# Kernel tuning notes

Measured on AMD Instinct MI355X. Metric: run time of the kernel, lower is better.

Reference implementation:

```python
import jax, jax.numpy as jnp
import numpy as np

B, L, K, H = 256, 256, 128, 256


def setup_inputs() -> dict:
    key = jax.random.key(0)
    ks = jax.random.split(key, 24)

    def u(k, shape, fan):
        s = 1.0 / np.sqrt(fan)
        return jax.random.uniform(k, shape, minval=-s, maxval=s, dtype=jnp.float32)

    x = jax.random.normal(ks[0], (B, L, K), jnp.float32)
    mask = (jax.random.uniform(ks[1], (B, L, K)) < 0.7).astype(jnp.float32)
    record_num = jax.random.randint(ks[2], (B,), L // 2, L + 1)
    ts = jnp.cumsum(jax.random.uniform(ks[3], (B, L), minval=0.1, maxval=1.0, dtype=jnp.float32), axis=1)
    time_stamp = ts * (jnp.arange(L)[None, :] < record_num[:, None]).astype(jnp.float32)

    return {
        "x": x,
        "mask": mask,
        "time_stamp": time_stamp,
        # TemporalDecay h: W [H,K], stdv = 1/sqrt(out)=1/sqrt(H)
        "W_gh": u(ks[4], (H, K), H), "b_gh": u(ks[5], (H,), H),
        # TemporalDecay x (diag): W [K,K], stdv = 1/sqrt(K)
        "W_gx": u(ks[6], (K, K), K), "b_gx": u(ks[7], (K,), K),
        # hist_reg: Linear(H -> K), stdv = 1/sqrt(H)
        "W_hist": u(ks[8], (K, H), H), "b_hist": u(ks[9], (K,), H),
        "W_feat": u(ks[10], (K, K), K), "b_feat": u(ks[11], (K,), K),
        # weight_combine: Linear(2K -> K), stdv = 1/sqrt(2K)
        "W_comb": u(ks[12], (K, 2 * K), 2 * K), "b_comb": u(ks[13], (K,), 2 * K),
        # GRUCell(2K -> H): uniform 1/sqrt(H)
        "W_ih": u(ks[14], (3 * H, 2 * K), H), "W_hh": u(ks[15], (3 * H, H), H),
        "b_ih": u(ks[16], (3 * H,), H), "b_hh": u(ks[17], (3 * H,), H),
        # out: Linear(H -> 1)
        "W_out": u(ks[18], (1, H), H), "b_out": u(ks[19], (1,), H),
        "record_num": record_num,
        "direct": 0,
    }


def _forward(x, mask, time_stamp, W_gh, b_gh, W_gx, b_gx, W_hist, b_hist,
             W_feat, b_feat, W_comb, b_comb, W_ih, W_hh, b_ih, b_hh,
             W_out, b_out, record_num):
    Bs, Ls, Ks = x.shape
    Hs = W_gh.shape[0]
    eye = jnp.eye(Ks, dtype=x.dtype)
    W_gx_m = W_gx * eye                 # diag temporal decay
    W_feat_m = W_feat * (1.0 - eye)

    # --- deltas (gen_aux_data): d[0]=1; d[t] = |ts[t]-ts[t-1]| + (1-m[t])*d[t-1] ---
    gaps = jnp.abs(jnp.diff(time_stamp, axis=1))          # [B, L-1]
    mask_t = jnp.swapaxes(mask, 0, 1)                     # [L, B, K]

    def dstep(prev, inp):
        gap, m = inp                                      # [B], [B,K]
        d = gap[:, None] + (1.0 - m) * prev
        return d, d

    d0 = jnp.ones((Bs, Ks), x.dtype)
    _, drest = jax.lax.scan(dstep, d0, (gaps.T, mask_t[1:]))
    deltas = jnp.concatenate([d0[None], drest], axis=0)   # [L, B, K]
    valid = (jnp.arange(Ls)[:, None] < record_num[None, :])  # break at record_num
    deltas = jnp.where(valid[:, :, None], deltas, 0.0)

    evals = (time_stamp != 0).astype(x.dtype)             # [B, L]

    x_t = jnp.swapaxes(x, 0, 1)                           # [L, B, K]
    e_t = evals.T                                         # [L, B]

    def step(carry, inp):
        h, xloss = carry
        xt, mt, dt, et = inp                              # [B,K],[B,K],[B,K],[B]
        e_m = et[:, None]
        gamma_h = jnp.exp(-jax.nn.relu(dt @ W_gh.T + b_gh))   # [B,H]
        gamma_x = jnp.exp(-jax.nn.relu(dt @ W_gx_m.T + b_gx)) # [B,K]
        h_prev = h
        h = h * gamma_h
        x_h = h @ W_hist.T + b_hist
        msum = jnp.sum(mt) + 1e-5
        xloss = xloss + jnp.sum(jnp.abs(xt - x_h) * mt) / msum
        x_c = mt * xt + (1.0 - mt) * x_h
        z_h = x_c @ W_feat_m.T + b_feat
        xloss = xloss + jnp.sum(jnp.abs(xt - z_h) * mt * e_m) / msum
        alpha = jnp.concatenate([gamma_x, mt], axis=1) @ W_comb.T + b_comb
        c_h = alpha * z_h + (1.0 - alpha) * x_h
        xloss = xloss + jnp.sum(jnp.abs(xt - c_h) * mt * e_m) / msum
        c_c = mt * xt + (1.0 - mt) * c_h
        inputs = jnp.concatenate([c_c, mt], axis=1)           # [B, 2K]
        gi = inputs @ W_ih.T + b_ih                           # [B, 3H]
        gh = h @ W_hh.T + b_hh
        ir, iz, ig = jnp.split(gi, 3, axis=1)
        hr, hz, hg = jnp.split(gh, 3, axis=1)
        r = jax.nn.sigmoid(ir + hr)
        z = jax.nn.sigmoid(iz + hz)
        n = jnp.tanh(ig + r * hg)
        h_new = (1.0 - z) * n + z * h
        h_new = h_new * e_m + (1.0 - e_m) * h_prev            # freeze h past record
        return (h_new, xloss), c_c * e_m

    h0 = jnp.zeros((Bs, Hs), x.dtype)
    (h_fin, x_loss), imps = jax.lax.scan(step, (h0, jnp.float32(0.0)), (x_t, mask_t, deltas, e_t))
    imputations = jnp.swapaxes(imps, 0, 1)                # [B, L, K]
    predictions = jax.nn.sigmoid(h_fin @ W_out.T + b_out) # [B, 1]
    return imputations, x_loss, predictions


def reference(x, mask, time_stamp, W_gh, b_gh, W_gx, b_gx, W_hist, b_hist,
              W_feat, b_feat, W_comb, b_comb, W_ih, W_hh, b_ih, b_hh,
              W_out, b_out, record_num, direct):
    return _forward(x, mask, time_stamp, W_gh, b_gh, W_gx, b_gx, W_hist, b_hist,
                    W_feat, b_feat, W_comb, b_comb, W_ih, W_hh, b_ih, b_hh,
                    W_out, b_out, record_num)
```

## Files before the change

### kernel.cpp

```cpp
#include <hip/hip_runtime.h>
#include <math.h>

#define BT 256
#define LT 256
#define KT 128
#define HT 256
#define LOSS_IDX ((size_t)BT*LT*KT)
#define PRED_IDX (LOSS_IDX + 1)
#define LDP 1280
#define GH0 0
#define AL0 256
#define GI0 384
#define ZP0 1152

typedef _Float16 h2 __attribute__((ext_vector_type(2)));
typedef _Float16 f16x8 __attribute__((ext_vector_type(8)));
typedef float f32x4 __attribute__((ext_vector_type(4)));

__device__ __forceinline__ float fd2(h2 a, h2 b, float c){
#if __has_builtin(__builtin_amdgcn_fdot2)
  return __builtin_amdgcn_fdot2(a, b, c, false);
#else
  return c + (float)a[0]*(float)b[0] + (float)a[1]*(float)b[1];
#endif
}
__device__ __forceinline__ h2 lo2(f16x8 v){ return __builtin_shufflevector(v,v,0,1); }
__device__ __forceinline__ h2 p1(f16x8 v){ return __builtin_shufflevector(v,v,2,3); }
__device__ __forceinline__ h2 p2(f16x8 v){ return __builtin_shufflevector(v,v,4,5); }
__device__ __forceinline__ h2 p3(f16x8 v){ return __builtin_shufflevector(v,v,6,7); }
__device__ __forceinline__ float sigf(float v){ return 1.0f/(1.0f + __expf(-v)); }
__device__ __forceinline__ float tanh_fast(float v){
  float a = fminf(fabsf(v), 15.0f);
  float e2 = __expf(2.0f*a);
  float r = (e2 - 1.0f)/(e2 + 1.0f);
  return copysignf(r, v);
}
__device__ __forceinline__ float f16bits(unsigned u, int hi){
  union { unsigned short s; _Float16 h; } c;
  c.s = (unsigned short)(hi ? (u >> 16) : (u & 0xffff));
  return (float)c.h;
}

__global__ void pack_cast(const float* __restrict__ src, _Float16* __restrict__ dst,
                          int J, int Kd, int diag, int total){
  int idx = blockIdx.x*256 + threadIdx.x;
  if (idx >= total) return;
  float v = src[idx];
  if (diag && (idx / Kd) == (idx % Kd)) v = 0.0f;
  dst[idx] = (_Float16)v;
}
__global__ void pack_rowchunks(const float* __restrict__ src, _Float16* __restrict__ dst,
                               int J, int K, int total){
  int idx = blockIdx.x*256 + threadIdx.x;
  if (idx >= total) return;
  int j = idx % J, c = idx / J;
  #pragma unroll
  for (int e = 0; e < 8; ++e)
    dst[(size_t)idx*8 + e] = (_Float16)src[(size_t)j*K + c*8 + e];
}
__global__ void pack_col(const float* __restrict__ src, _Float16* __restrict__ dst,
                         int J, int Kc, int ld, int diag, int total){
  int idx = blockIdx.x*256 + threadIdx.x;
  if (idx >= total) return;
  int j = idx % J, k = idx / J;
  float v = src[(size_t)j*ld + k];
  if (diag && j == k) v = 0.0f;
  dst[idx] = (_Float16)v;
}

__global__ __launch_bounds__(128) void scan_kernel(
    const float* __restrict__ x, const float* __restrict__ mask, const float* __restrict__ ts,
    const float* __restrict__ W_gx, const float* __restrict__ b_gx,
    const int* __restrict__ record_num,
    _Float16* __restrict__ deltas, _Float16* __restrict__ Agx, _Float16* __restrict__ U)
{
  int b = blockIdx.x, k = threadIdx.x;
  int rn = record_num[b];
  float gxd = W_gx[(size_t)k*KT + k];
  float bgx = b_gx[k];
  float d = 1.0f, tsp = 0.0f;
  for (int t0 = 0; t0 < LT; t0 += 8){
    float xv[8], mv[8], tsv[8];
    #pragma unroll
    for (int u = 0; u < 8; ++u){
      size_t off = ((size_t)b*LT + t0 + u)*KT + k;
      xv[u] = x[off]; mv[u] = mask[off];
      tsv[u] = ts[(size_t)b*LT + t0 + u];
    }
    #pragma unroll
    for (int u = 0; u < 8; ++u){
      int t = t0 + u;
      if (t > 0){
        float gap = fabsf(tsv[u] - (u ? tsv[u-1] : tsp));
        d = gap + (1.0f - mv[u])*d;
      }
      float e = (t < rn) ? 1.0f : 0.0f;
      float dev = d * e;
      size_t row = (size_t)b*LT + t;
      deltas[row*KT + k] = (_Float16)dev;
      float gx = __expf(-fmaxf(fmaf(dev, gxd, bgx), 0.0f));
      Agx[row*2*KT + k]      = (_Float16)gx;
      Agx[row*2*KT + KT + k] = (_Float16)mv[u];
      U[row*2*KT + k]        = (_Float16)(mv[u]*xv[u]);
      U[row*2*KT + KT + k]   = (_Float16)mv[u];
    }
    tsp = tsv[7];
  }
}

__global__ void msum_kernel(const float* __restrict__ mask, float* __restrict__ msumInv){
  __shared__ float red[256];
  int t = blockIdx.x;
  float acc = 0.0f;
  for (int i = threadIdx.x; i < BT*KT; i += 256){
    int b = i >> 7, k = i & 127;
    acc += mask[((size_t)b*LT + t)*KT + k];
  }
  red[threadIdx.x] = acc; __syncthreads();
  for (int s = 128; s > 0; s >>= 1){
    if (threadIdx.x < s) red[threadIdx.x] += red[threadIdx.x + s];
    __syncthreads();
  }
  if (threadIdx.x == 0) msumInv[t] = 1.0f/(red[0] + 1e-5f);
}

__global__ __launch_bounds__(256) void gemm_f16(
    const _Float16* __restrict__ A, long ldA, int K,
    const _Float16* __restrict__ B, long ldB,
    _Float16* __restrict__ C, long colofs,
    const float* __restrict__ bias, int op)
{
  const int w = threadIdx.x >> 6, lane = threadIdx.x & 63;
  const int ml = lane & 15, quad = lane >> 4;
  const long m0 = (long)blockIdx.x*64 + w*16;
  const long nb0 = (long)blockIdx.y*64;
  f32x4 acc[4] = {{0,0,0,0},{0,0,0,0},{0,0,0,0},{0,0,0,0}};
  for (int kc = 0; kc < K; kc += 32){
    f16x8 a = *(const f16x8*)(A + (m0 + ml)*ldA + kc + quad*8);
    #pragma unroll
    for (int nt = 0; nt < 4; ++nt){
      f16x8 bfr = *(const f16x8*)(B + (nb0 + nt*16 + ml)*ldB + kc + quad*8);
      acc[nt] = __builtin_amdgcn_mfma_f32_16x16x32_f16(a, bfr, acc[nt], 0, 0, 0);
    }
  }
  #pragma unroll
  for (int nt = 0; nt < 4; ++nt){
    long col = nb0 + nt*16 + ml;
    float bv = (op >= 1) ? bias[col] : 0.0f;
    #pragma unroll
    for (int r = 0; r < 4; ++r){
      float v = acc[nt][r];
      if (op >= 1) v += bv;
      if (op == 2) v = __expf(-fmaxf(v, 0.0f));
      long row = m0 + quad*4 + r;
      C[row*LDP + colofs + col] = (_Float16)v;
    }
  }
}

#define NT 1024

struct __align__(16) SeqS {
  f16x8 whist_l[32*128];
  _Float16 wfc_l[128*128];
  float h[HT];
  float hs[HT];
  alignas(16) _Float16 hsh[HT];
  float gh[3*HT];
  float gi[3*HT];
  float xh[KT];
  float v3[136];
  alignas(4) _Float16 v5h[136];
  int lidx[136];
  int posk[KT];
  int cnt;
  unsigned gam[2][128];
  unsigned pbd[2][512];
  float xb[2][KT], mb[2][KT];
  float bhist[KT], bfeat[KT];
  float bhh[3*HT];
  float wout[HT];
  float minv[LT];
  float red[NT/64];
};

__global__ __launch_bounds__(NT, 1) void rits_seq(
    const float* __restrict__ x, const float* __restrict__ mask,
    const int* __restrict__ record_num, const float* __restrict__ msumInv,
    const _Float16* __restrict__ P,
    const f16x8* __restrict__ Whh_p, const f16x8* __restrict__ Whist_p,
    const _Float16* __restrict__ Wfc, const _Float16* __restrict__ Wihc,
    const float* __restrict__ b_hist, const float* __restrict__ b_feat,
    const float* __restrict__ b_hh,
    const float* __restrict__ W_out, const float* __restrict__ b_out,
    float* __restrict__ out)
{
  __shared__ SeqS s;
  const int tid = threadIdx.x;
  const int b = blockIdx.x;
  const int rn = record_num[b];
  const unsigned* __restrict__ Pd = (const unsigned*)P + (size_t)b*LT*(LDP/2);

  for (int i = tid; i < 32*128; i += NT) s.whist_l[i] = Whist_p[i];
  for (int i = tid; i < 128*128/2; i += NT)
    ((unsigned*)s.wfc_l)[i] = ((const unsigned*)Wfc)[i];
  if (tid < HT){ s.h[tid] = 0.0f; s.hs[tid] = 0.0f; s.hsh[tid] = (_Float16)0.0f; }
  if (tid < KT){ s.bhist[tid] = b_hist[tid]; s.bfeat[tid] = b_feat[tid]; }
  if (tid < 3*HT) s.bhh[tid] = b_hh[tid];
  if (tid < 136) s.lidx[tid] = 0;
  if (tid >= 768 && tid < 768 + HT) s.wout[tid - 768] = W_out[tid - 768];
  if (tid >= 512 && tid < 512 + LT) s.minv[tid - 512] = msumInv[tid - 512];
  if (tid == 0) s.cnt = 0;
  if (tid < 128) s.gam[0][tid] = Pd[tid];
  if (tid >= 256 && tid < 768) s.pbd[0][tid - 256] = Pd[128 + tid - 256];
  if (tid >= 896){
    int k = tid - 896;
    s.xb[0][k] = x[((size_t)b*LT)*KT + k];
    s.mb[0][k] = mask[((size_t)b*LT)*KT + k];
  }
  __syncthreads();

  float loss = 0.0f;
  unsigned pr[5]; float prx = 0.0f, prm = 0.0f;
  h2 wpre[16];

  for (int t = 0; t < LT; ++t){
    const int cur = t & 1, nxt = cur ^ 1;
    const int last = (t == LT - 1);

    if (tid < 768){
      const f16x8* hp = (const f16x8*)s.hsh;
      float a0=0.f, a1=0.f, a2=0.f, a3=0.f;
      #pragma unroll
      for (int c = 0; c < 32; ++c){
        f16x8 w = Whh_p[c*768 + tid];
        f16x8 av = hp[c];
        a0 = fd2(lo2(w), lo2(av), a0);
        a1 = fd2(p1(w),  p1(av),  a1);
        a2 = fd2(p2(w),  p2(av),  a2);
        a3 = fd2(p3(w),  p3(av),  a3);
      }
      s.gh[tid] = (a0 + a1) + (a2 + a3);
    } else if (tid < 896){
      const int j = tid - 768;
      const f16x8* hp = (const f16x8*)s.hsh;
      float a0=0.f, a1=0.f, a2=0.f, a3=0.f;
      #pragma unroll
      for (int c = 0; c < 32; ++c){
        f16x8 w = s.whist_l[c*128 + j];
        f16x8 av = hp[c];
        a0 = fd2(lo2(w), lo2(av), a0);
        a1 = fd2(p1(w),  p1(av),  a1);
        a2 = fd2(p2(w),  p2(av),  a2);
        a3 = fd2(p3(w),  p3(av),  a3);
      }
      float xh = (a0 + a1) + (a2 + a3) + s.bhist[j];
      s.xh[j] = xh;
      float mv = s.mb[cur][j], xv = s.xb[cur][j];
      loss += fabsf(xv - xh) * mv * s.minv[t];
      bool miss = (mv == 0.0f);
      unsigned long long bal = __ballot(miss);
      int lane = tid & 63;
      int rank = __popcll(bal & ((1ull << lane) - 1ull));
      int wcnt = __popcll(bal);
      int base = 0;
      if (lane == 0 && wcnt) base = atomicAdd(&s.cnt, wcnt);
      base = __shfl(base, 0);
      if (miss){
        int pp = base + rank;
        s.lidx[pp] = j; s.v3[pp] = xh; s.posk[j] = pp;
      }
    } else {
      if (!last){
        int i = tid - 896;
        const unsigned* Pn = Pd + (size_t)(t + 1)*(LDP/2);
        #pragma unroll
        for (int u = 0; u < 5; ++u) pr[u] = Pn[u*128 + i];
        size_t offx = ((size_t)b*LT + t + 1)*KT + i;
        prx = x[offx]; prm = mask[offx];
      }
    }
    __syncthreads();

    const int c0 = s.cnt;
    if (tid < 768){
      #pragma unroll
      for (int u = 0; u < 16; ++u){
        h2 w;
        w[0] = Wihc[(size_t)s.lidx[2*u]*768 + tid];
        w[1] = Wihc[(size_t)s.lidx[2*u + 1]*768 + tid];
        wpre[u] = w;
      }
    }
    if (tid < KT){
      const int j = tid;
      float za = 0.0f, zb = 0.0f;
      int i = 0;
      for (; i + 1 < c0; i += 2){
        za += s.v3[i]     * (float)s.wfc_l[s.lidx[i]*128 + j];
        zb += s.v3[i + 1] * (float)s.wfc_l[s.lidx[i + 1]*128 + j];
      }
      if (i < c0) za += s.v3[i] * (float)s.wfc_l[s.lidx[i]*128 + j];
      float z = f16bits(s.pbd[cur][448 + (j >> 1)], j & 1) + s.bfeat[j] + za + zb;
      float al = f16bits(s.pbd[cur][j >> 1], j & 1);
      float xh = s.xh[j];
      float mv = s.mb[cur][j], xv = s.xb[cur][j];
      float e = (t < rn) ? 1.0f : 0.0f;
      float inv = s.minv[t];
      float ch = al*z + (1.0f - al)*xh;
      loss += (fabsf(xv - z) + fabsf(xv - ch)) * mv * e * inv;
      float cc = mv*xv + (1.0f - mv)*ch;
      out[((size_t)b*LT + t)*KT + j] = cc * e;
      if (mv == 0.0f) s.v5h[s.posk[j]] = (_Float16)ch;
    } else if (tid < 168){
      int i2 = c0 + (tid - 128);
      if (i2 < 136) s.v5h[i2] = (_Float16)0.0f;
    }
    if (tid >= 896 && !last) s.gam[nxt][tid - 896] = pr[0];
    __syncthreads();

    if (tid < 768){
      float g  = f16bits(s.pbd[cur][64 + (tid >> 1)], tid & 1);
      float g2 = 0.0f;
      const h2* v5p = (const h2*)s.v5h;
      #pragma unroll
      for (int u = 0; u < 16; u += 2){
        g  = fd2(wpre[u],     v5p[u],     g);
        g2 = fd2(wpre[u + 1], v5p[u + 1], g2);
      }
      for (int i = 32; i < c0; ++i)
        g2 += (float)s.v5h[i] * (float)Wihc[(size_t)s.lidx[i]*768 + tid];
      s.gi[tid] = g + g2;
    }
    __syncthreads();

    if (tid < HT){
      const int j = tid;
      float ir = s.gi[j], iz = s.gi[HT + j], ig = s.gi[2*HT + j];
      float hr = s.gh[j] + s.bhh[j];
      float hz = s.gh[HT + j] + s.bhh[HT + j];
      float hg = s.gh[2*HT + j] + s.bhh[2*HT + j];
      float r = sigf(ir + hr);
      float zg = sigf(iz + hz);
      float n = tanh_fast(ig + r*hg);
      float hscur = s.hs[j];
      float hn = (1.0f - zg)*n + zg*hscur;
      float he = (t < rn) ? hn : s.h[j];
      s.h[j] = he;
      if (!last){
        float gn = f16bits(s.gam[nxt][j >> 1], j & 1);
        float hsn = he * gn;
        s.hs[j] = hsn;
        s.hsh[j] = (_Float16)hsn;
      }
    }
    if (tid == HT) s.cnt = 0;
    if (tid >= 896 && !last){
      int i = tid - 896;
      #pragma unroll
      for (int u = 1; u < 5; ++u) s.pbd[nxt][(u - 1)*128 + i] = pr[u];
      s.xb[nxt][i] = prx; s.mb[nxt][i] = prm;
    }
    __syncthreads();
  }

  #pragma unroll
  for (int off = 32; off; off >>= 1) loss += __shfl_down(loss, off);
  if ((tid & 63) == 0) s.red[tid >> 6] = loss;
  __syncthreads();
  if (tid == 0){
    float tot = 0.0f;
    #pragma unroll
    for (int w = 0; w < NT/64; ++w) tot += s.red[w];
    atomicAdd(&out[LOSS_IDX], tot);
  }

  if (tid < HT) s.gh[tid] = s.h[tid] * s.wout[tid];
  __syncthreads();
  for (int st2 = 128; st2 > 0; st2 >>= 1){
    if (tid < st2) s.gh[tid] += s.gh[tid + st2];
    __syncthreads();
  }
  if (tid == 0) out[PRED_IDX + b] = sigf(s.gh[0] + b_out[0]);
}

extern "C" void kernel_launch(void* const* d_in, const int* in_sizes, int n_in,
                              void* d_out, int out_size, void* d_ws, size_t ws_size,
                              hipStream_t stream){
  const float* x      = (const float*)d_in[0];
  const float* mask   = (const float*)d_in[1];
  const float* ts     = (const float*)d_in[2];
  const float* W_gh   = (const float*)d_in[3];
  const float* b_gh   = (const float*)d_in[4];
  const float* W_gx   = (const float*)d_in[5];
  const float* b_gx   = (const float*)d_in[6];
  const float* W_hist = (const float*)d_in[7];
  const float* b_hist = (const float*)d_in[8];
  const float* W_feat = (const float*)d_in[9];
  const float* b_feat = (const float*)d_in[10];
  const float* W_comb = (const float*)d_in[11];
  const float* b_comb = (const float*)d_in[12];
  const float* W_ih   = (const float*)d_in[13];
  const float* W_hh   = (const float*)d_in[14];
  const float* b_ih   = (const float*)d_in[15];
  const float* b_hh   = (const float*)d_in[16];
  const float* W_out  = (const float*)d_in[17];
  const float* b_out  = (const float*)d_in[18];
  const int*   rn     = (const int*)d_in[19];
  float* out = (float*)d_out;
  char* ws = (char*)d_ws;

  size_t off = 0;
  auto alloc = [&](size_t bytes) -> char* {
    char* p = ws + off;
    off += (bytes + 255) & ~(size_t)255;
    return p;
  };
  _Float16* P      = (_Float16*)alloc((size_t)BT*LT*LDP*2);
  _Float16* deltas = (_Float16*)alloc((size_t)BT*LT*KT*2);
  _Float16* Agx    = (_Float16*)alloc((size_t)BT*LT*2*KT*2);
  _Float16* U      = (_Float16*)alloc((size_t)BT*LT*2*KT*2);
  _Float16* WghF   = (_Float16*)alloc(HT*KT*2);
  _Float16* WcombF = (_Float16*)alloc(KT*2*KT*2);
  _Float16* WihF   = (_Float16*)alloc(3*HT*2*KT*2);
  _Float16* WfeatF = (_Float16*)alloc(KT*KT*2);
  _Float16* Whh_p  = (_Float16*)alloc(3*HT*HT*2);
  _Float16* Whist_p= (_Float16*)alloc(KT*HT*2);
  _Float16* Wfc    = (_Float16*)alloc(KT*KT*2);
  _Float16* Wihc   = (_Float16*)alloc(KT*3*HT*2);
  float* msumInv   = (float*)alloc(LT*4);

  auto grid1 = [](int n){ return dim3((n + 255)/256); };
  pack_cast<<<grid1(HT*KT), 256, 0, stream>>>(W_gh, WghF, HT, KT, 0, HT*KT);
  pack_cast<<<grid1(KT*2*KT), 256, 0, stream>>>(W_comb, WcombF, KT, 2*KT, 0, KT*2*KT);
  pack_cast<<<grid1(3*HT*2*KT), 256, 0, stream>>>(W_ih, WihF, 3*HT, 2*KT, 0, 3*HT*2*KT);
  pack_cast<<<grid1(KT*KT), 256, 0, stream>>>(W_feat, WfeatF, KT, KT, 1, KT*KT);
  pack_rowchunks<<<grid1(3*HT*(HT/8)), 256, 0, stream>>>(W_hh, Whh_p, 3*HT, HT, 3*HT*(HT/8));
  pack_rowchunks<<<grid1(KT*(HT/8)), 256, 0, stream>>>(W_hist, Whist_p, KT, HT, KT*(HT/8));
  pack_col<<<grid1(KT*KT), 256, 0, stream>>>(W_feat, Wfc, KT, KT, KT, 1, KT*KT);
  pack_col<<<grid1(768*KT), 256, 0, stream>>>(W_ih, Wihc, 3*HT, KT, 2*KT, 0, 3*HT*KT);

  scan_kernel<<<dim3(BT), dim3(KT), 0, stream>>>(x, mask, ts, W_gx, b_gx, rn, deltas, Agx, U);
  msum_kernel<<<dim3(LT), dim3(256), 0, stream>>>(mask, msumInv);

  const int MR = BT*LT;
  gemm_f16<<<dim3(MR/64, HT/64), 256, 0, stream>>>(deltas, KT, KT, WghF, KT, P, GH0, b_gh, 2);
  gemm_f16<<<dim3(MR/64, KT/64), 256, 0, stream>>>(Agx, 2*KT, 2*KT, WcombF, 2*KT, P, AL0, b_comb, 1);
  gemm_f16<<<dim3(MR/64, 3*HT/64), 256, 0, stream>>>(U, 2*KT, 2*KT, WihF, 2*KT, P, GI0, b_ih, 1);
  gemm_f16<<<dim3(MR/64, KT/64), 256, 0, stream>>>(U, 2*KT, KT, WfeatF, KT, P, ZP0, (const float*)nullptr, 0);

  hipMemsetAsync((void*)(out + LOSS_IDX), 0, sizeof(float), stream);

  rits_seq<<<dim3(BT), dim3(NT), 0, stream>>>(x, mask, rn, msumInv, P,
      (const f16x8*)Whh_p, (const f16x8*)Whist_p, Wfc, Wihc,
      b_hist, b_feat, b_hh, W_out, b_out, out);
}
```

Baseline: 2.692 ms.

## Collapse per-step recurrence into one wavefront critical path with fewer barriers

Restructures the sequential RITS kernel so a single 64-thread wavefront computes the history regression, feature regression, combine and sparse input-gate update for all 128 features, while the other waves compute the hidden-gate matvec in parallel. This cuts the per-timestep barriers from four to two and removes the shared atomic counter by using in-wave ballots. W_ih columns are repacked as pairs to suit the new per-thread access, and prefetch of the next step's data is written directly to shared memory. The exchange is that the serial chain now runs on one wave with more work per thread, which may lengthen the critical path when many features are missing.

```diff
diff --git a/kernel.cpp b/kernel.cpp
--- a/kernel.cpp
+++ b/kernel.cpp
@@ -25,9 +25,9 @@
 #endif
 }
 __device__ __forceinline__ h2 lo2(f16x8 v){ return __builtin_shufflevector(v,v,0,1); }
-__device__ __forceinline__ h2 p1(f16x8 v){ return __builtin_shufflevector(v,v,2,3); }
-__device__ __forceinline__ h2 p2(f16x8 v){ return __builtin_shufflevector(v,v,4,5); }
-__device__ __forceinline__ h2 p3(f16x8 v){ return __builtin_shufflevector(v,v,6,7); }
+__device__ __forceinline__ h2 p1v(f16x8 v){ return __builtin_shufflevector(v,v,2,3); }
+__device__ __forceinline__ h2 p2v(f16x8 v){ return __builtin_shufflevector(v,v,4,5); }
+__device__ __forceinline__ h2 p3v(f16x8 v){ return __builtin_shufflevector(v,v,6,7); }
 __device__ __forceinline__ float sigf(float v){ return 1.0f/(1.0f + __expf(-v)); }
 __device__ __forceinline__ float tanh_fast(float v){
   float a = fminf(fabsf(v), 15.0f);
@@ -66,6 +66,14 @@
   float v = src[(size_t)j*ld + k];
   if (diag && j == k) v = 0.0f;
   dst[idx] = (_Float16)v;
+}
+__global__ void pack_colpair(const float* __restrict__ src, _Float16* __restrict__ dst,
+                             int total){
+  int idx = blockIdx.x*256 + threadIdx.x;
+  if (idx >= total) return;
+  int k = idx / 384, m = idx % 384;
+  dst[(size_t)2*idx]     = (_Float16)src[(size_t)m*(2*KT) + k];
+  dst[(size_t)2*idx + 1] = (_Float16)src[(size_t)(m + 384)*(2*KT) + k];
 }
 
 __global__ __launch_bounds__(128) void scan_kernel(
@@ -158,33 +166,29 @@
   }
 }
 
-#define NT 1024
+#define NTS 1024
 
 struct __align__(16) SeqS {
   f16x8 whist_l[32*128];
-  _Float16 wfc_l[128*128];
+  h2 wfcp[128*64];
   float h[HT];
   float hs[HT];
   alignas(16) _Float16 hsh[HT];
   float gh[3*HT];
   float gi[3*HT];
-  float xh[KT];
-  float v3[136];
-  alignas(4) _Float16 v5h[136];
-  int lidx[136];
-  int posk[KT];
-  int cnt;
-  unsigned gam[2][128];
+  float v3[KT];
+  float v5[KT];
+  int lidx[KT];
+  unsigned gam[128];
   unsigned pbd[2][512];
   float xb[2][KT], mb[2][KT];
   float bhist[KT], bfeat[KT];
   float bhh[3*HT];
   float wout[HT];
   float minv[LT];
-  float red[NT/64];
 };
 
-__global__ __launch_bounds__(NT, 1) void rits_seq(
+__global__ __launch_bounds__(NTS) void rits_seq(
     const float* __restrict__ x, const float* __restrict__ mask,
     const int* __restrict__ record_num, const float* __restrict__ msumInv,
     const _Float16* __restrict__ P,
@@ -201,136 +205,150 @@
   const int rn = record_num[b];
   const unsigned* __restrict__ Pd = (const unsigned*)P + (size_t)b*LT*(LDP/2);
 
-  for (int i = tid; i < 32*128; i += NT) s.whist_l[i] = Whist_p[i];
-  for (int i = tid; i < 128*128/2; i += NT)
-    ((unsigned*)s.wfc_l)[i] = ((const unsigned*)Wfc)[i];
-  if (tid < HT){ s.h[tid] = 0.0f; s.hs[tid] = 0.0f; s.hsh[tid] = (_Float16)0.0f; }
+  for (int i = tid; i < 32*128; i += NTS) s.whist_l[i] = Whist_p[i];
+  for (int i = tid; i < 128*64; i += NTS){
+    int k = i >> 6, l = i & 63;
+    h2 w; w[0] = Wfc[k*128 + l]; w[1] = Wfc[k*128 + 64 + l];
+    s.wfcp[i] = w;
+  }
+  if (tid < HT){ s.h[tid] = 0.0f; s.hs[tid] = 0.0f; s.hsh[tid] = (_Float16)0.0f;
+                 s.wout[tid] = W_out[tid]; }
   if (tid < KT){ s.bhist[tid] = b_hist[tid]; s.bfeat[tid] = b_feat[tid]; }
-  if (tid < 3*HT) s.bhh[tid] = b_hh[tid];
-  if (tid < 136) s.lidx[tid] = 0;
-  if (tid >= 768 && tid < 768 + HT) s.wout[tid - 768] = W_out[tid - 768];
-  if (tid >= 512 && tid < 512 + LT) s.minv[tid - 512] = msumInv[tid - 512];
-  if (tid == 0) s.cnt = 0;
-  if (tid < 128) s.gam[0][tid] = Pd[tid];
-  if (tid >= 256 && tid < 768) s.pbd[0][tid - 256] = Pd[128 + tid - 256];
-  if (tid >= 896){
-    int k = tid - 896;
+  if (tid >= 256 && tid < 256 + 3*HT) s.bhh[tid - 256] = b_hh[tid - 256];
+  if (tid >= 64 && tid < 576) s.pbd[0][tid - 64] = Pd[128 + (tid - 64)];
+  if (tid >= 576 && tid < 704){
+    int k = tid - 576;
     s.xb[0][k] = x[((size_t)b*LT)*KT + k];
     s.mb[0][k] = mask[((size_t)b*LT)*KT + k];
   }
+  if (tid >= 704 && tid < 960) s.minv[tid - 704] = msumInv[tid - 704];
   __syncthreads();
 
   float loss = 0.0f;
-  unsigned pr[5]; float prx = 0.0f, prm = 0.0f;
-  h2 wpre[16];
 
   for (int t = 0; t < LT; ++t){
     const int cur = t & 1, nxt = cur ^ 1;
     const int last = (t == LT - 1);
 
-    if (tid < 768){
+    if (tid < 64){
+      const int j0 = tid, j1 = tid + 64;
+      const float inv = s.minv[t];
+      float mv0 = s.mb[cur][j0], mv1 = s.mb[cur][j1];
+      float xv0 = s.xb[cur][j0], xv1 = s.xb[cur][j1];
+      bool miss0 = (mv0 == 0.0f), miss1 = (mv1 == 0.0f);
+      unsigned long long bal0 = __ballot(miss0);
+      unsigned long long bal1 = __ballot(miss1);
+      unsigned long long ltm = (1ull << tid) - 1ull;
+      int cA = __popcll(bal0);
+      int c0 = cA + __popcll(bal1);
+      int pos0 = __popcll(bal0 & ltm);
+      int pos1 = cA + __popcll(bal1 & ltm);
+      if (miss0) s.lidx[pos0] = j0;
+      if (miss1) s.lidx[pos1] = j1;
+      const f16x8* hp = (const f16x8*)s.hsh;
+      float A0=0.f,A1=0.f,A2=0.f,A3=0.f,B0=0.f,B1=0.f,B2=0.f,B3=0.f;
+      #pragma unroll 8
+      for (int c = 0; c < 32; ++c){
+        f16x8 av = hp[c];
+        f16x8 w0 = s.whist_l[c*128 + j0];
+        f16x8 w1 = s.whist_l[c*128 + j1];
+        A0 = fd2(lo2(w0), lo2(av), A0); A1 = fd2(p1v(w0), p1v(av), A1);
+        A2 = fd2(p2v(w0), p2v(av), A2); A3 = fd2(p3v(w0), p3v(av), A3);
+        B0 = fd2(lo2(w1), lo2(av), B0); B1 = fd2(p1v(w1), p1v(av), B1);
+        B2 = fd2(p2v(w1), p2v(av), B2); B3 = fd2(p3v(w1), p3v(av), B3);
+      }
+      float xh0 = (A0+A1)+(A2+A3) + s.bhist[j0];
+      float xh1 = (B0+B1)+(B2+B3) + s.bhist[j1];
+      loss += (fabsf(xv0 - xh0)*mv0 + fabsf(xv1 - xh1)*mv1) * inv;
+      if (miss0) s.v3[pos0] = xh0;
+      if (miss1) s.v3[pos1] = xh1;
+      float za0=0.f, za1=0.f, zb0=0.f, zb1=0.f;
+      {
+        int i = 0;
+        for (; i + 1 < c0; i += 2){
+          int l0 = s.lidx[i], l1 = s.lidx[i + 1];
+          float v0 = s.v3[i], v1 = s.v3[i + 1];
+          h2 wa = s.wfcp[l0*64 + tid];
+          h2 wb = s.wfcp[l1*64 + tid];
+          za0 += v0*(float)wa[0]; za1 += v0*(float)wa[1];
+          zb0 += v1*(float)wb[0]; zb1 += v1*(float)wb[1];
+        }
+        if (i < c0){
+          int l0 = s.lidx[i]; float v0 = s.v3[i];
+          h2 wa = s.wfcp[l0*64 + tid];
+          za0 += v0*(float)wa[0]; za1 += v0*(float)wa[1];
+        }
+      }
+      float z0 = f16bits(s.pbd[cur][448 + (j0 >> 1)], j0 & 1) + s.bfeat[j0] + za0 + zb0;
+      float z1 = f16bits(s.pbd[cur][448 + (j1 >> 1)], j1 & 1) + s.bfeat[j1] + za1 + zb1;
+      float al0 = f16bits(s.pbd[cur][j0 >> 1], j0 & 1);
+      float al1 = f16bits(s.pbd[cur][j1 >> 1], j1 & 1);
+      float e = (t < rn) ? 1.0f : 0.0f;
+      float ch0 = al0*z0 + (1.0f - al0)*xh0;
+      float ch1 = al1*z1 + (1.0f - al1)*xh1;
+      loss += ((fabsf(xv0 - z0) + fabsf(xv0 - ch0))*mv0
+             + (fabsf(xv1 - z1) + fabsf(xv1 - ch1))*mv1) * e * inv;
+      float cc0 = mv0*xv0 + (1.0f - mv0)*ch0;
+      float cc1 = mv1*xv1 + (1.0f - mv1)*ch1;
+      out[((size_t)b*LT + t)*KT + j0] = cc0 * e;
+      out[((size_t)b*LT + t)*KT + j1] = cc1 * e;
+      if (miss0) s.v5[pos0] = ch0;
+      if (miss1) s.v5[pos1] = ch1;
+      float g[12];
+      #pragma unroll
+      for (int u = 0; u < 6; ++u){
+        int m = tid + 64*u;
+        g[u]     = f16bits(s.pbd[cur][64 + (m >> 1)], m & 1);
+        int m2 = m + 384;
+        g[6 + u] = f16bits(s.pbd[cur][64 + (m2 >> 1)], m2 & 1);
+      }
+      for (int i = 0; i < c0; ++i){
+        float vv = s.v5[i];
+        const h2* wr = (const h2*)(Wihc + (size_t)s.lidx[i]*768);
+        #pragma unroll
+        for (int u = 0; u < 6; ++u){
+          h2 w = wr[tid + 64*u];
+          g[u]     += vv*(float)w[0];
+          g[6 + u] += vv*(float)w[1];
+        }
+      }
+      #pragma unroll
+      for (int u = 0; u < 6; ++u){
+        s.gi[tid + 64*u]       = g[u];
+        s.gi[384 + tid + 64*u] = g[6 + u];
+      }
+    } else if (tid < 832) {
+      const int gj = tid - 64;
       const f16x8* hp = (const f16x8*)s.hsh;
       float a0=0.f, a1=0.f, a2=0.f, a3=0.f;
-      #pragma unroll
+      #pragma unroll 8
       for (int c = 0; c < 32; ++c){
-        f16x8 w = Whh_p[c*768 + tid];
+        f16x8 w = Whh_p[c*768 + gj];
         f16x8 av = hp[c];
         a0 = fd2(lo2(w), lo2(av), a0);
-        a1 = fd2(p1(w),  p1(av),  a1);
-        a2 = fd2(p2(w),  p2(av),  a2);
-        a3 = fd2(p3(w),  p3(av),  a3);
-      }
-      s.gh[tid] = (a0 + a1) + (a2 + a3);
-    } else if (tid < 896){
-      const int j = tid - 768;
-      const f16x8* hp = (const f16x8*)s.hsh;
-      float a0=0.f, a1=0.f, a2=0.f, a3=0.f;
-      #pragma unroll
-      for (int c = 0; c < 32; ++c){
-        f16x8 w = s.whist_l[c*128 + j];
-        f16x8 av = hp[c];
-        a0 = fd2(lo2(w), lo2(av), a0);
-        a1 = fd2(p1(w),  p1(av),  a1);
-        a2 = fd2(p2(w),  p2(av),  a2);
-        a3 = fd2(p3(w),  p3(av),  a3);
-      }
-      float xh = (a0 + a1) + (a2 + a3) + s.bhist[j];
-      s.xh[j] = xh;
-      float mv = s.mb[cur][j], xv = s.xb[cur][j];
-      loss += fabsf(xv - xh) * mv * s.minv[t];
-      bool miss = (mv == 0.0f);
-      unsigned long long bal = __ballot(miss);
-      int lane = tid & 63;
-      int rank = __popcll(bal & ((1ull << lane) - 1ull));
-      int wcnt = __popcll(bal);
-      int base = 0;
-      if (lane == 0 && wcnt) base = atomicAdd(&s.cnt, wcnt);
-      base = __shfl(base, 0);
-      if (miss){
-        int pp = base + rank;
-        s.lidx[pp] = j; s.v3[pp] = xh; s.posk[j] = pp;
-      }
+        a1 = fd2(p1v(w), p1v(av), a1);
+        a2 = fd2(p2v(w), p2v(av), a2);
+        a3 = fd2(p3v(w), p3v(av), a3);
+      }
+      s.gh[gj] = (a0 + a1) + (a2 + a3);
     } else {
       if (!last){
-        int i = tid - 896;
+        int pf = tid - 832;
         const unsigned* Pn = Pd + (size_t)(t + 1)*(LDP/2);
-        #pragma unroll
-        for (int u = 0; u < 5; ++u) pr[u] = Pn[u*128 + i];
-        size_t offx = ((size_t)b*LT + t + 1)*KT + i;
-        prx = x[offx]; prm = mask[offx];
-      }
-    }
-    __syncthreads();
-
-    const int c0 = s.cnt;
-    if (tid < 768){
-      #pragma unroll
-      for (int u = 0; u < 16; ++u){
-        h2 w;
-        w[0] = Wihc[(size_t)s.lidx[2*u]*768 + tid];
-        w[1] = Wihc[(size_t)s.lidx[2*u + 1]*768 + tid];
-        wpre[u] = w;
-      }
-    }
-    if (tid < KT){
-      const int j = tid;
-      float za = 0.0f, zb = 0.0f;
-      int i = 0;
-      for (; i + 1 < c0; i += 2){
-        za += s.v3[i]     * (float)s.wfc_l[s.lidx[i]*128 + j];
-        zb += s.v3[i + 1] * (float)s.wfc_l[s.lidx[i + 1]*128 + j];
-      }
-      if (i < c0) za += s.v3[i] * (float)s.wfc_l[s.lidx[i]*128 + j];
-      float z = f16bits(s.pbd[cur][448 + (j >> 1)], j & 1) + s.bfeat[j] + za + zb;
-      float al = f16bits(s.pbd[cur][j >> 1], j & 1);
-      float xh = s.xh[j];
-      float mv = s.mb[cur][j], xv = s.xb[cur][j];
-      float e = (t < rn) ? 1.0f : 0.0f;
-      float inv = s.minv[t];
-      float ch = al*z + (1.0f - al)*xh;
-      loss += (fabsf(xv - z) + fabsf(xv - ch)) * mv * e * inv;
-      float cc = mv*xv + (1.0f - mv)*ch;
-      out[((size_t)b*LT + t)*KT + j] = cc * e;
-      if (mv == 0.0f) s.v5h[s.posk[j]] = (_Float16)ch;
-    } else if (tid < 168){
-      int i2 = c0 + (tid - 128);
-      if (i2 < 136) s.v5h[i2] = (_Float16)0.0f;
-    }
-    if (tid >= 896 && !last) s.gam[nxt][tid - 896] = pr[0];
-    __syncthreads();
-
-    if (tid < 768){
-      float g  = f16bits(s.pbd[cur][64 + (tid >> 1)], tid & 1);
-      float g2 = 0.0f;
-      const h2* v5p = (const h2*)s.v5h;
-      #pragma unroll
-      for (int u = 0; u < 16; u += 2){
-        g  = fd2(wpre[u],     v5p[u],     g);
-        g2 = fd2(wpre[u + 1], v5p[u + 1], g2);
-      }
-      for (int i = 32; i < c0; ++i)
-        g2 += (float)s.v5h[i] * (float)Wihc[(size_t)s.lidx[i]*768 + tid];
-      s.gi[tid] = g + g2;
+        if (pf < 128){
+          s.gam[pf] = Pn[pf];
+          #pragma unroll
+          for (int u = 0; u < 4; ++u)
+            s.pbd[nxt][u*128 + pf] = Pn[128 + u*128 + pf];
+        } else {
+          int k2 = pf - 128;
+          const float2* xp = (const float2*)(x + ((size_t)b*LT + t + 1)*KT);
+          const float2* mp = (const float2*)(mask + ((size_t)b*LT + t + 1)*KT);
+          float2 xv = xp[k2], mv = mp[k2];
+          s.xb[nxt][2*k2] = xv.x;   s.xb[nxt][2*k2 + 1] = xv.y;
+          s.mb[nxt][2*k2] = mv.x;   s.mb[nxt][2*k2 + 1] = mv.y;
+        }
+      }
     }
     __syncthreads();
 
@@ -343,45 +361,32 @@
       float r = sigf(ir + hr);
       float zg = sigf(iz + hz);
       float n = tanh_fast(ig + r*hg);
-      float hscur = s.hs[j];
-      float hn = (1.0f - zg)*n + zg*hscur;
+      float hn = (1.0f - zg)*n + zg*s.hs[j];
       float he = (t < rn) ? hn : s.h[j];
       s.h[j] = he;
       if (!last){
-        float gn = f16bits(s.gam[nxt][j >> 1], j & 1);
+        float gn = f16bits(s.gam[j >> 1], j & 1);
         float hsn = he * gn;
         s.hs[j] = hsn;
         s.hsh[j] = (_Float16)hsn;
       }
     }
-    if (tid == HT) s.cnt = 0;
-    if (tid >= 896 && !last){
-      int i = tid - 896;
-      #pragma unroll
-      for (int u = 1; u < 5; ++u) s.pbd[nxt][(u - 1)*128 + i] = pr[u];
-      s.xb[nxt][i] = prx; s.mb[nxt][i] = prm;
-    }
     __syncthreads();
   }
 
-  #pragma unroll
-  for (int off = 32; off; off >>= 1) loss += __shfl_down(loss, off);
-  if ((tid & 63) == 0) s.red[tid >> 6] = loss;
-  __syncthreads();
-  if (tid == 0){
-    float tot = 0.0f;
+  if (tid < 64){
     #pragma unroll
-    for (int w = 0; w < NT/64; ++w) tot += s.red[w];
-    atomicAdd(&out[LOSS_IDX], tot);
-  }
-
-  if (tid < HT) s.gh[tid] = s.h[tid] * s.wout[tid];
+    for (int off = 32; off; off >>= 1) loss += __shfl_down(loss, off);
+    if (tid == 0) atomicAdd(&out[LOSS_IDX], loss);
+  }
+
+  if (tid < HT) s.gi[tid] = s.h[tid] * s.wout[tid];
   __syncthreads();
   for (int st2 = 128; st2 > 0; st2 >>= 1){
-    if (tid < st2) s.gh[tid] += s.gh[tid + st2];
+    if (tid < st2) s.gi[tid] += s.gi[tid + st2];
     __syncthreads();
   }
-  if (tid == 0) out[PRED_IDX + b] = sigf(s.gh[0] + b_out[0]);
+  if (tid == 0) out[PRED_IDX + b] = sigf(s.gi[0] + b_out[0]);
 }
 
 extern "C" void kernel_launch(void* const* d_in, const int* in_sizes, int n_in,
@@ -438,7 +443,7 @@
   pack_rowchunks<<<grid1(3*HT*(HT/8)), 256, 0, stream>>>(W_hh, Whh_p, 3*HT, HT, 3*HT*(HT/8));
   pack_rowchunks<<<grid1(KT*(HT/8)), 256, 0, stream>>>(W_hist, Whist_p, KT, HT, KT*(HT/8));
   pack_col<<<grid1(KT*KT), 256, 0, stream>>>(W_feat, Wfc, KT, KT, KT, 1, KT*KT);
-  pack_col<<<grid1(768*KT), 256, 0, stream>>>(W_ih, Wihc, 3*HT, KT, 2*KT, 0, 3*HT*KT);
+  pack_colpair<<<grid1(KT*384), 256, 0, stream>>>(W_ih, Wihc, KT*384);
 
   scan_kernel<<<dim3(BT), dim3(KT), 0, stream>>>(x, mask, ts, W_gx, b_gx, rn, deltas, Agx, U);
   msum_kernel<<<dim3(LT), dim3(256), 0, stream>>>(mask, msumInv);
@@ -451,7 +456,7 @@
 
   hipMemsetAsync((void*)(out + LOSS_IDX), 0, sizeof(float), stream);
 
-  rits_seq<<<dim3(BT), dim3(NT), 0, stream>>>(x, mask, rn, msumInv, P,
+  rits_seq<<<dim3(BT), dim3(NTS), 0, stream>>>(x, mask, rn, msumInv, P,
       (const f16x8*)Whh_p, (const f16x8*)Whist_p, Wfc, Wihc,
       b_hist, b_feat, b_hh, W_out, b_out, out);
 }
```

Result: faster. 2.493 ms (-7.4%).
